# Performance work log

Hardware: AMD Instinct MI355X
Metric: run time of the kernel (lower is better)

## Reference

```python
import jax, jax.numpy as jnp
import numpy as np

B, C, H, W = 8, 128, 64, 64
D_STATE = 16
D_CONV = 4
EXPAND = 1.25
D_INNER = int(EXPAND * C)        # 160
DT_RANK = int(np.ceil(C / 16))   # 8


def setup_inputs() -> dict:
    key = jax.random.key(0)
    ks = jax.random.split(key, 10)
    f = lambda k, s, sc=0.02: jax.random.normal(k, s, dtype=jnp.float32) * sc
    return {
        "x": jax.random.normal(ks[0], (B, C, H, W), dtype=jnp.float32),
        "ln_g": jnp.ones((C,), jnp.float32),
        "ln_b": jnp.zeros((C,), jnp.float32),
        "in_proj_w": f(ks[1], (2 * D_INNER, C)),
        "conv_w": f(ks[2], (D_INNER, 1, D_CONV)),            # depthwise causal conv kernel
        "conv_b": jnp.zeros((D_INNER,), jnp.float32),
        "x_proj_w": f(ks[3], (DT_RANK + 2 * D_STATE, D_INNER)),
        "dt_proj_w": f(ks[4], (D_INNER, DT_RANK), 0.1),
        "dt_proj_b": f(ks[5], (D_INNER,), 0.1),
        # S4-style init: A_log = log(1..d_state) per inner channel (frozen in torch module)
        "A_log": jnp.log(jnp.tile(jnp.arange(1, D_STATE + 1, dtype=jnp.float32), (D_INNER, 1))),
        "D_param": jnp.ones((D_INNER,), jnp.float32),
        "out_proj_w": f(ks[6], (C, D_INNER)),
        "fuse_w": f(ks[7], (C, 2 * C)),                      # 1x1 conv == per-token matmul
        "scale": jnp.ones((1,), jnp.float32) * 0.1,
    }


def _layernorm(x, g, b, eps=1e-5):
    m = x.mean(-1, keepdims=True)
    v = x.var(-1, keepdims=True)
    return (x - m) * jax.lax.rsqrt(v + eps) * g + b


def _mamba(seq, in_proj_w, conv_w, conv_b, x_proj_w, dt_proj_w, dt_proj_b,
           A_log, D_param, out_proj_w):
    # seq: (B, L, C)
    Bsz, L, _ = seq.shape
    xz = jnp.einsum('blc,ec->ble', seq, in_proj_w)           # (B, L, 2*d_inner)
    xm, z = jnp.split(xz, 2, axis=-1)
    # depthwise causal conv over L, truncated to L (padding = d_conv-1 on the left)
    xc = jax.lax.conv_general_dilated(
        xm.transpose(0, 2, 1), conv_w, (1,), [(D_CONV - 1, 0)],
        feature_group_count=D_INNER, dimension_numbers=('NCH', 'OIH', 'NCH'))
    xm = jax.nn.silu((xc + conv_b[None, :, None]).transpose(0, 2, 1))  # (B, L, d_inner)
    x_dbl = jnp.einsum('bld,ed->ble', xm, x_proj_w)
    dt = x_dbl[..., :DT_RANK]
    Bm = x_dbl[..., DT_RANK:DT_RANK + D_STATE]               # (B, L, d_state)
    Cm = x_dbl[..., DT_RANK + D_STATE:]                      # (B, L, d_state)
    dt = jax.nn.softplus(jnp.einsum('blr,dr->bld', dt, dt_proj_w) + dt_proj_b)
    A = -jnp.exp(A_log)                                      # (d_inner, d_state)

    def step(h, inp):
        dt_t, B_t, C_t, x_t = inp                            # (B,d) (B,n) (B,n) (B,d)
        dA = jnp.exp(dt_t[:, :, None] * A)                   # (B, d_inner, d_state)
        h = dA * h + (dt_t * x_t)[:, :, None] * B_t[:, None, :]
        y = jnp.einsum('bdn,bn->bd', h, C_t)
        return h, y

    h0 = jnp.zeros((Bsz, D_INNER, D_STATE), dtype=seq.dtype)
    xs = (dt.transpose(1, 0, 2), Bm.transpose(1, 0, 2),
          Cm.transpose(1, 0, 2), xm.transpose(1, 0, 2))
    _, ys = jax.lax.scan(step, h0, xs)                       # ys: (L, B, d_inner)
    y = ys.transpose(1, 0, 2) + xm * D_param
    y = y * jax.nn.silu(z)
    return jnp.einsum('bld,cd->blc', y, out_proj_w)          # (B, L, C)


def reference(x, ln_g, ln_b, in_proj_w, conv_w, conv_b, x_proj_w, dt_proj_w,
              dt_proj_b, A_log, D_param, out_proj_w, fuse_w, scale):
    Bsz, Ch, Hh, Ww = x.shape
    seq = x.reshape(Bsz, Ch, Hh * Ww).transpose(0, 2, 1)     # (B, L, C) raster order
    seq_n = _layernorm(seq, ln_g, ln_b)                      # LN is per-token: commutes with flip
    args = (in_proj_w, conv_w, conv_b, x_proj_w, dt_proj_w, dt_proj_b,
            A_log, D_param, out_proj_w)
    y0 = _mamba(seq_n, *args)                                # forward raster scan
    y1 = _mamba(seq_n[:, ::-1, :], *args)[:, ::-1, :]        # reversed raster scan
    fused = jnp.einsum('blk,ck->blc', jnp.concatenate([y0, y1], axis=-1), fuse_w)
    out = seq + scale * fused                                # residual + learned scale
    return out.transpose(0, 2, 1).reshape(Bsz, Ch, Hh, Ww)
```

## Files before the change

kernel.cpp:

```cpp
#include <hip/hip_runtime.h>
#include <math.h>

#define LSEQ   4096
#define BATCH  8
#define CDIM   128
#define DIN    160
#define DSTATE 16
#define DTRANK 8
#define BLROWS (BATCH*LSEQ)
#define NCHUNK 128
#define TCH    32
#define SUBC   8
#define NSEG   16

typedef __attribute__((ext_vector_type(8))) short short8;
typedef __attribute__((ext_vector_type(8))) __bf16 bf16x8;
typedef __attribute__((ext_vector_type(4))) float float4v;

__device__ __forceinline__ float4v mfma_bf16(short8 a, short8 b, float4v c) {
  return __builtin_amdgcn_mfma_f32_16x16x32_bf16(
      __builtin_bit_cast(bf16x8, a), __builtin_bit_cast(bf16x8, b), c, 0, 0, 0);
}

__device__ __forceinline__ unsigned short f2bf(float f) {
  union { float f; unsigned u; } v; v.f = f;
  unsigned r = v.u + 0x7FFF + ((v.u >> 16) & 1);
  return (unsigned short)(r >> 16);
}
__device__ __forceinline__ float bf2f(unsigned short h) {
  union { unsigned u; float f; } v; v.u = ((unsigned)h) << 16;
  return v.f;
}

__global__ void prep_weights(const float* __restrict__ inpw, const float* __restrict__ xpw,
                             const float* __restrict__ fuse_w, const float* __restrict__ out_proj_w,
                             unsigned short* __restrict__ inpw_bf, unsigned short* __restrict__ xpw_bf,
                             unsigned short* __restrict__ W01) {
  int i = blockIdx.x * 256 + threadIdx.x;
  if (i < 320 * 128) inpw_bf[i] = f2bf(inpw[i]);
  if (i < 40 * 160)  xpw_bf[i]  = f2bf(xpw[i]);
  if (i < CDIM * DIN) {
    int d = i % DIN, c = i / DIN;
    float a0 = 0.f, a1 = 0.f;
    for (int k = 0; k < CDIM; ++k) {
      float o = out_proj_w[k * DIN + d];
      a0 += fuse_w[c * 256 + k] * o;
      a1 += fuse_w[c * 256 + 128 + k] * o;
    }
    W01[c * DIN + d] = f2bf(a0);
    W01[CDIM * DIN + c * DIN + d] = f2bf(a1);
  }
}

__global__ void ln_transpose_kernel(const float* __restrict__ x,
                                    const float* __restrict__ g,
                                    const float* __restrict__ bb,
                                    unsigned short* __restrict__ seqn) {
  __shared__ float sA[128 * 65];
  __shared__ float psum[2 * 256];
  __shared__ float mrs[2 * 64];
  int l0 = blockIdx.x * 64;
  int b  = blockIdx.y;
  int t  = threadIdx.x;
  int lsub = t & 63, crow = t >> 6;
  const float* xb = x + (size_t)b * CDIM * LSEQ;
  for (int it = 0; it < 32; ++it) {
    int c = crow + it * 4;
    sA[c * 65 + lsub] = xb[(size_t)c * LSEQ + l0 + lsub];
  }
  __syncthreads();
  float s = 0.f, ss = 0.f;
  for (int j = 0; j < 32; ++j) {
    int c = crow * 32 + j;
    float v = sA[c * 65 + lsub];
    s += v; ss += v * v;
  }
  psum[crow * 64 + lsub] = s;
  psum[256 + crow * 64 + lsub] = ss;
  __syncthreads();
  if (t < 64) {
    float su = 0.f, sq = 0.f;
    for (int p = 0; p < 4; ++p) { su += psum[p * 64 + t]; sq += psum[256 + p * 64 + t]; }
    float m = su * (1.f / 128.f);
    float var = sq * (1.f / 128.f) - m * m;
    mrs[t] = m;
    mrs[64 + t] = rsqrtf(var + 1e-5f);
  }
  __syncthreads();
  int c = t & 127, half = t >> 7;
  float gc = g[c], bc = bb[c];
  for (int it = 0; it < 32; ++it) {
    int l = it * 2 + half;
    float v = (sA[c * 65 + l] - mrs[l]) * mrs[64 + l] * gc + bc;
    seqn[((size_t)(b * LSEQ + l0 + l)) * CDIM + c] = f2bf(v);
  }
}

template<int K, bool MASKN, bool BF16OUT>
__global__ __launch_bounds__(256)
void gemm_mfma(const unsigned short* __restrict__ A0, const unsigned short* __restrict__ A1,
               const unsigned short* __restrict__ W,
               void* __restrict__ C0, void* __restrict__ C1, int N) {
  constexpr int LSTR = K + 8;
  __shared__ __align__(16) unsigned short As[64 * LSTR];
  __shared__ __align__(16) unsigned short Ws[64 * LSTR];
  const unsigned short* A = blockIdx.z ? A1 : A0;
  void* Cp = blockIdx.z ? C1 : C0;
  int m0 = blockIdx.x * 64;
  int n0 = blockIdx.y * 64;
  int t = threadIdx.x;
  constexpr int CH = 64 * K / 8;
  for (int c = t; c < CH; c += 256) {
    int row = c / (K / 8);
    int col = (c % (K / 8)) * 8;
    *(short8*)&As[row * LSTR + col] = *(const short8*)&A[(size_t)(m0 + row) * K + col];
    short8 wv = {};
    int nr = n0 + row;
    if (!MASKN || nr < N) wv = *(const short8*)&W[(size_t)nr * K + col];
    *(short8*)&Ws[row * LSTR + col] = wv;
  }
  __syncthreads();
  int lane = t & 63;
  int w = t >> 6;
  int l15 = lane & 15, quad = lane >> 4;
  float4v acc[4] = {};
#pragma unroll
  for (int kk = 0; kk < K; kk += 32) {
    short8 bfrag = *(const short8*)&Ws[(w * 16 + l15) * LSTR + kk + quad * 8];
#pragma unroll
    for (int i = 0; i < 4; ++i) {
      short8 afrag = *(const short8*)&As[(i * 16 + l15) * LSTR + kk + quad * 8];
      acc[i] = mfma_bf16(afrag, bfrag, acc[i]);
    }
  }
  int col = n0 + w * 16 + l15;
  if (MASKN && col >= N) return;
#pragma unroll
  for (int i = 0; i < 4; ++i)
#pragma unroll
    for (int r = 0; r < 4; ++r) {
      int row = m0 + i * 16 + quad * 4 + r;
      if (BF16OUT) ((unsigned short*)Cp)[(size_t)row * N + col] = f2bf(acc[i][r]);
      else         ((float*)Cp)[(size_t)row * N + col] = acc[i][r];
    }
}

__global__ void conv_silu_kernel(const unsigned short* __restrict__ xz,
                                 const float* __restrict__ cw,
                                 const float* __restrict__ cb,
                                 unsigned short* __restrict__ xm0,
                                 unsigned short* __restrict__ xm1) {
  int idx = blockIdx.x * 256 + threadIdx.x;
  int dir = blockIdx.y;
  if (idx >= BLROWS * 80) return;
  int dp = idx % 80;
  int bl = idx / 80;
  int l = bl % LSEQ, b = bl / LSEQ;
  int d = dp * 2;
  float w0[4], w1[4];
#pragma unroll
  for (int k = 0; k < 4; ++k) { w0[k] = cw[d * 4 + k]; w1[k] = cw[d * 4 + 4 + k]; }
  float a0 = cb[d], a1 = cb[d + 1];
  const unsigned short* base = xz + ((size_t)b * LSEQ) * 320 + d;
  if (dir == 0) {
#pragma unroll
    for (int k = 0; k < 4; ++k) {
      int lp = l - 3 + k;
      if (lp >= 0) {
        unsigned v = *(const unsigned*)&base[(size_t)lp * 320];
        a0 += w0[k] * bf2f((unsigned short)v);
        a1 += w1[k] * bf2f((unsigned short)(v >> 16));
      }
    }
  } else {
#pragma unroll
    for (int k = 0; k < 4; ++k) {
      int lp = l + 3 - k;
      if (lp < LSEQ) {
        unsigned v = *(const unsigned*)&base[(size_t)lp * 320];
        a0 += w0[k] * bf2f((unsigned short)v);
        a1 += w1[k] * bf2f((unsigned short)(v >> 16));
      }
    }
  }
  float s0 = a0 / (1.f + __expf(-a0));
  float s1 = a1 / (1.f + __expf(-a1));
  unsigned outv = (unsigned)f2bf(s0) | ((unsigned)f2bf(s1) << 16);
  unsigned short* xm = dir ? xm1 : xm0;
  *(unsigned*)&xm[(size_t)bl * DIN + d] = outv;
}

__device__ __forceinline__ void decay_powers(float r1, float* dA) {
  float r2 = r1 * r1;
  float r4 = r2 * r2;
  float r8 = r4 * r4;
  dA[0] = r1;       dA[1] = r2;       dA[2] = r2 * r1;  dA[3] = r4;
  dA[4] = r4 * r1;  dA[5] = r4 * r2;  dA[6] = r4 * dA[2]; dA[7] = r8;
  dA[8] = r8 * r1;  dA[9] = r8 * r2;  dA[10] = r8 * dA[2]; dA[11] = r8 * r4;
  dA[12] = r8 * dA[4]; dA[13] = r8 * dA[5]; dA[14] = r8 * dA[6]; dA[15] = r8 * r8;
}

__device__ __forceinline__ const float* uniform_row(const float* base, int elem_off) {
  return base + __builtin_amdgcn_readfirstlane(elem_off);
}

__global__ void scan_passA(const float* __restrict__ xdbl0, const float* __restrict__ xdbl1,
                           const unsigned short* __restrict__ xm0v, const unsigned short* __restrict__ xm1v,
                           const float* __restrict__ dt_w, const float* __restrict__ dt_b,
                           const float* __restrict__ Dp,
                           float* __restrict__ Q, float* __restrict__ dtsum,
                           _Float16* __restrict__ rc0, _Float16* __restrict__ rc1,
                           unsigned short* __restrict__ y0, unsigned short* __restrict__ y1) {
  int chunk = blockIdx.x, b = blockIdx.y, dir = blockIdx.z;
  int t = threadIdx.x;
  if (t >= DIN) return;
  const float* xdbl = dir ? xdbl1 : xdbl0;
  const unsigned short* xm = dir ? xm1v : xm0v;
  _Float16* rc = dir ? rc1 : rc0;
  unsigned short* yl = dir ? y1 : y0;
  int d = t;
  float dw[8];
#pragma unroll
  for (int r = 0; r < 8; ++r) dw[r] = dt_w[d * 8 + r];
  float db = dt_b[d];
  float Dd = Dp[d];
  float h[16];
#pragma unroll
  for (int n = 0; n < 16; ++n) h[n] = 0.f;
  float cum = 0.f;
  float rcum = 1.f;
#pragma unroll 4
  for (int tt = 0; tt < TCH; ++tt) {
    int pos = chunk * TCH + tt;
    int l = dir ? (LSEQ - 1 - pos) : pos;
    int rowi = b * LSEQ + l;
    const float* xr = uniform_row(xdbl, rowi * 40);
    float xmv = bf2f(xm[(size_t)rowi * DIN + d]);
    float zz = db;
#pragma unroll
    for (int r = 0; r < 8; ++r) zz += xr[r] * dw[r];
    float e  = __expf(fminf(zz, 20.f));
    float dt = (zz > 20.f) ? zz : __logf(1.f + e);
    float r1 = 1.f / (1.f + e);
    cum += dt;
    rcum *= r1;
    rc[(size_t)rowi * DIN + d] = (_Float16)rcum;
    float u = dt * xmv;
    float dA[16];
    decay_powers(r1, dA);
    float y = xmv * Dd;
#pragma unroll
    for (int n = 0; n < 16; ++n) {
      h[n] = dA[n] * h[n] + u * xr[8 + n];
      y += h[n] * xr[24 + n];
    }
    yl[(size_t)rowi * DIN + d] = f2bf(y);
  }
  size_t base = (size_t)((dir * BATCH + b) * NCHUNK + chunk);
#pragma unroll
  for (int n = 0; n < 16; ++n) Q[base * (DIN * 16) + d * 16 + n] = h[n];
  dtsum[base * DIN + d] = cum;
}

__global__ __launch_bounds__(256)
void scan_passB(const float* __restrict__ Q, const float* __restrict__ dtsum,
                float* __restrict__ Hinit) {
  __shared__ float sA[NSEG * 16], sQ[NSEG * 16];
  int blk = blockIdx.x;
  int d = blk % DIN;
  int rem = blk / DIN;
  int t = threadIdx.x;
  int n = t & 15, cs = t >> 4;
  float An = -(float)(n + 1);
  float a[SUBC], q[SUBC];
  float Aseg = 1.f, Qseg = 0.f;
#pragma unroll
  for (int j = 0; j < SUBC; ++j) {
    int ch = cs * SUBC + j;
    size_t base = (size_t)rem * NCHUNK + ch;
    float dsv = dtsum[base * DIN + d];
    float av = __expf(An * dsv);
    float qv = Q[base * (DIN * 16) + d * 16 + n];
    a[j] = av; q[j] = qv;
    Qseg = av * Qseg + qv;
    Aseg *= av;
  }
  sA[cs * 16 + n] = Aseg;
  sQ[cs * 16 + n] = Qseg;
  __syncthreads();
  if (t < 16) {
    float h = 0.f;
    for (int s = 0; s < NSEG; ++s) {
      float Av = sA[s * 16 + t], Qv = sQ[s * 16 + t];
      sA[s * 16 + t] = h;
      h = Av * h + Qv;
    }
  }
  __syncthreads();
  float h = sA[cs * 16 + n];
#pragma unroll
  for (int j = 0; j < SUBC; ++j) {
    int ch = cs * SUBC + j;
    size_t base = (size_t)rem * NCHUNK + ch;
    Hinit[base * (DIN * 16) + d * 16 + n] = h;
    h = a[j] * h + q[j];
  }
}

__global__ void scan_passC(const float* __restrict__ xdbl0, const float* __restrict__ xdbl1,
                           const unsigned short* __restrict__ xz,
                           const float* __restrict__ Hinit,
                           const _Float16* __restrict__ rc0, const _Float16* __restrict__ rc1,
                           const unsigned short* __restrict__ yl0, const unsigned short* __restrict__ yl1,
                           unsigned short* __restrict__ yg0, unsigned short* __restrict__ yg1) {
  int chunk = blockIdx.x, b = blockIdx.y, dir = blockIdx.z;
  int t = threadIdx.x;
  if (t >= DIN) return;
  const float* xdbl = dir ? xdbl1 : xdbl0;
  const _Float16* rc = dir ? rc1 : rc0;
  const unsigned short* yl = dir ? yl1 : yl0;
  unsigned short* yg = dir ? yg1 : yg0;
  int d = t;
  size_t base = (size_t)((dir * BATCH + b) * NCHUNK + chunk);
  float H0[16];
#pragma unroll
  for (int n = 0; n < 16; ++n) H0[n] = Hinit[base * (DIN * 16) + d * 16 + n];
#pragma unroll 2
  for (int tt = 0; tt < TCH; ++tt) {
    int pos = chunk * TCH + tt;
    int l = dir ? (LSEQ - 1 - pos) : pos;
    int rowi = b * LSEQ + l;
    const float* xr = uniform_row(xdbl, rowi * 40 + 24);
    size_t di = (size_t)rowi * DIN + d;
    float y = bf2f(yl[di]);
    float rcum = (float)rc[di];
    float zv = bf2f(xz[(size_t)rowi * 320 + 160 + d]);
    float dA[16];
    decay_powers(rcum, dA);
    float corr = 0.f;
#pragma unroll
    for (int n = 0; n < 16; ++n) corr += xr[n] * dA[n] * H0[n];
    y += corr;
    float sz = zv / (1.f + __expf(-zv));
    yg[di] = f2bf(y * sz);
  }
}

__global__ __launch_bounds__(256)
void final_mfma(const unsigned short* __restrict__ yg0, const unsigned short* __restrict__ yg1,
                const unsigned short* __restrict__ W01, const float* __restrict__ x,
                const float* __restrict__ scale, float* __restrict__ out) {
  constexpr int K = DIN, LSTR = K + 8;
  __shared__ __align__(16) unsigned short As[64 * LSTR];
  __shared__ __align__(16) unsigned short Ws[64 * LSTR];
  float* sC = (float*)As;
  int m0 = blockIdx.x * 64;
  int c0 = blockIdx.y * 64;
  int b = m0 / LSEQ, l0 = m0 % LSEQ;
  int t = threadIdx.x;
  int lane = t & 63;
  int w = t >> 6;
  int l15 = lane & 15, quad = lane >> 4;
  float4v acc[4] = {};
  for (int pass = 0; pass < 2; ++pass) {
    const unsigned short* A = pass ? yg1 : yg0;
    const unsigned short* W = W01 + pass * (CDIM * K);
    if (pass) __syncthreads();
    constexpr int CH = 64 * K / 8;
    for (int c = t; c < CH; c += 256) {
      int row = c / (K / 8);
      int col = (c % (K / 8)) * 8;
      *(short8*)&As[row * LSTR + col] = *(const short8*)&A[(size_t)(m0 + row) * K + col];
      *(short8*)&Ws[row * LSTR + col] = *(const short8*)&W[(size_t)(c0 + row) * K + col];
    }
    __syncthreads();
#pragma unroll
    for (int kk = 0; kk < K; kk += 32) {
      short8 bfrag = *(const short8*)&Ws[(w * 16 + l15) * LSTR + kk + quad * 8];
#pragma unroll
      for (int i = 0; i < 4; ++i) {
        short8 afrag = *(const short8*)&As[(i * 16 + l15) * LSTR + kk + quad * 8];
        acc[i] = mfma_bf16(afrag, bfrag, acc[i]);
      }
    }
  }
  __syncthreads();
#pragma unroll
  for (int i = 0; i < 4; ++i)
#pragma unroll
    for (int r = 0; r < 4; ++r)
      sC[(i * 16 + quad * 4 + r) * 65 + w * 16 + l15] = acc[i][r];
  __syncthreads();
  float sc = scale[0];
  int ll = t & 63, cq = t >> 6;
#pragma unroll
  for (int j = 0; j < 16; ++j) {
    int cl = cq * 16 + j;
    float v = sC[ll * 65 + cl];
    size_t gi = ((size_t)(b * CDIM + c0 + cl)) * LSEQ + l0 + ll;
    out[gi] = x[gi] + sc * v;
  }
}

extern "C" void kernel_launch(void* const* d_in, const int* in_sizes, int n_in,
                              void* d_out, int out_size, void* d_ws, size_t ws_size,
                              hipStream_t stream) {
  const float* x        = (const float*)d_in[0];
  const float* ln_g     = (const float*)d_in[1];
  const float* ln_b     = (const float*)d_in[2];
  const float* in_projw = (const float*)d_in[3];
  const float* conv_w   = (const float*)d_in[4];
  const float* conv_b   = (const float*)d_in[5];
  const float* x_projw  = (const float*)d_in[6];
  const float* dt_projw = (const float*)d_in[7];
  const float* dt_projb = (const float*)d_in[8];
  const float* A_log    = (const float*)d_in[9];
  const float* D_param  = (const float*)d_in[10];
  const float* out_projw= (const float*)d_in[11];
  const float* fuse_w   = (const float*)d_in[12];
  const float* scale    = (const float*)d_in[13];
  float* out = (float*)d_out;
  (void)A_log;

  float* ws = (float*)d_ws;
  size_t off = 0;
  unsigned short* seqn_bf = (unsigned short*)(ws + off); off += (size_t)BLROWS * CDIM / 2;
  unsigned short* xz      = (unsigned short*)(ws + off); off += (size_t)BLROWS * 320 / 2;
  unsigned short* xm0 = (unsigned short*)(ws + off); off += (size_t)BLROWS * DIN / 2;
  unsigned short* xm1 = (unsigned short*)(ws + off); off += (size_t)BLROWS * DIN / 2;
  float* xdbl0 = ws + off; off += (size_t)BLROWS * 40;
  float* xdbl1 = ws + off; off += (size_t)BLROWS * 40;
  float* Q     = ws + off; off += (size_t)2 * BATCH * NCHUNK * DIN * 16;
  float* Hinit = ws + off; off += (size_t)2 * BATCH * NCHUNK * DIN * 16;
  float* dtsum = ws + off; off += (size_t)2 * BATCH * NCHUNK * DIN;
  _Float16* rc0 = (_Float16*)(ws + off); off += (size_t)BLROWS * DIN / 2;
  _Float16* rc1 = (_Float16*)(ws + off); off += (size_t)BLROWS * DIN / 2;
  unsigned short* yl0 = (unsigned short*)(ws + off); off += (size_t)BLROWS * DIN / 2;
  unsigned short* yl1 = (unsigned short*)(ws + off); off += (size_t)BLROWS * DIN / 2;
  unsigned short* yg0 = (unsigned short*)(ws + off); off += (size_t)BLROWS * DIN / 2;
  unsigned short* yg1 = (unsigned short*)(ws + off); off += (size_t)BLROWS * DIN / 2;
  unsigned short* W01bf = (unsigned short*)(ws + off); off += (size_t)2 * CDIM * DIN / 2;
  unsigned short* inpw_bf = (unsigned short*)(ws + off); off += (size_t)320 * 128 / 2;
  unsigned short* xpw_bf  = (unsigned short*)(ws + off); off += (size_t)40 * 160 / 2 + 8;

  prep_weights<<<(320 * 128 + 255) / 256, 256, 0, stream>>>(
      in_projw, x_projw, fuse_w, out_projw, inpw_bf, xpw_bf, W01bf);
  ln_transpose_kernel<<<dim3(LSEQ / 64, BATCH), 256, 0, stream>>>(x, ln_g, ln_b, seqn_bf);
  gemm_mfma<128, false, true><<<dim3(BLROWS / 64, 5, 1), 256, 0, stream>>>(
      seqn_bf, seqn_bf, inpw_bf, xz, xz, 320);
  conv_silu_kernel<<<dim3((BLROWS * 80 + 255) / 256, 2), 256, 0, stream>>>(xz, conv_w, conv_b, xm0, xm1);
  gemm_mfma<160, true, false><<<dim3(BLROWS / 64, 1, 2), 256, 0, stream>>>(
      xm0, xm1, xpw_bf, xdbl0, xdbl1, 40);
  scan_passA<<<dim3(NCHUNK, BATCH, 2), 192, 0, stream>>>(xdbl0, xdbl1, xm0, xm1,
                                                         dt_projw, dt_projb, D_param,
                                                         Q, dtsum, rc0, rc1, yl0, yl1);
  scan_passB<<<2 * BATCH * DIN, 256, 0, stream>>>(Q, dtsum, Hinit);
  scan_passC<<<dim3(NCHUNK, BATCH, 2), 192, 0, stream>>>(xdbl0, xdbl1, xz, Hinit,
                                                         rc0, rc1, yl0, yl1, yg0, yg1);
  final_mfma<<<dim3(BLROWS / 64, CDIM / 64), 256, 0, stream>>>(yg0, yg1, W01bf, x, scale, out);
}
```

Measured before the change: 249.0 us.

## Halve scan chunk length, store chunk states in bf16, split correction reduction

Doubles the number of scan chunks (16 steps each instead of 32) so pass A and pass C launch twice as many blocks and each thread runs a shorter serial loop. Per-chunk end states Q and carried-in states Hinit are now stored as bf16 instead of fp32, which offsets the doubled state traffic. Pass C's 16-term correction sum is split into four independent accumulators to shorten the dependency chain. The cost is more inter-chunk state passing in pass B (16 sub-chunks per segment) and extra rounding error in the carried scan states.

```diff
diff --git a/kernel.cpp b/kernel.cpp
--- a/kernel.cpp
+++ b/kernel.cpp
@@ -8,9 +8,9 @@
 #define DSTATE 16
 #define DTRANK 8
 #define BLROWS (BATCH*LSEQ)
-#define NCHUNK 128
-#define TCH    32
-#define SUBC   8
+#define NCHUNK 256
+#define TCH    16
+#define SUBC   16
 #define NSEG   16
 
 typedef __attribute__((ext_vector_type(8))) short short8;
@@ -208,16 +208,16 @@
                            const unsigned short* __restrict__ xm0v, const unsigned short* __restrict__ xm1v,
                            const float* __restrict__ dt_w, const float* __restrict__ dt_b,
                            const float* __restrict__ Dp,
-                           float* __restrict__ Q, float* __restrict__ dtsum,
+                           unsigned short* __restrict__ Q, float* __restrict__ dtsum,
                            _Float16* __restrict__ rc0, _Float16* __restrict__ rc1,
-                           unsigned short* __restrict__ y0, unsigned short* __restrict__ y1) {
+                           unsigned short* __restrict__ y0out, unsigned short* __restrict__ y1out) {
   int chunk = blockIdx.x, b = blockIdx.y, dir = blockIdx.z;
   int t = threadIdx.x;
   if (t >= DIN) return;
   const float* xdbl = dir ? xdbl1 : xdbl0;
   const unsigned short* xm = dir ? xm1v : xm0v;
   _Float16* rc = dir ? rc1 : rc0;
-  unsigned short* yl = dir ? y1 : y0;
+  unsigned short* yl = dir ? y1out : y0out;
   int d = t;
   float dw[8];
 #pragma unroll
@@ -258,13 +258,13 @@
   }
   size_t base = (size_t)((dir * BATCH + b) * NCHUNK + chunk);
 #pragma unroll
-  for (int n = 0; n < 16; ++n) Q[base * (DIN * 16) + d * 16 + n] = h[n];
+  for (int n = 0; n < 16; ++n) Q[base * (DIN * 16) + d * 16 + n] = f2bf(h[n]);
   dtsum[base * DIN + d] = cum;
 }
 
 __global__ __launch_bounds__(256)
-void scan_passB(const float* __restrict__ Q, const float* __restrict__ dtsum,
-                float* __restrict__ Hinit) {
+void scan_passB(const unsigned short* __restrict__ Q, const float* __restrict__ dtsum,
+                unsigned short* __restrict__ Hinit) {
   __shared__ float sA[NSEG * 16], sQ[NSEG * 16];
   int blk = blockIdx.x;
   int d = blk % DIN;
@@ -280,7 +280,7 @@
     size_t base = (size_t)rem * NCHUNK + ch;
     float dsv = dtsum[base * DIN + d];
     float av = __expf(An * dsv);
-    float qv = Q[base * (DIN * 16) + d * 16 + n];
+    float qv = bf2f(Q[base * (DIN * 16) + d * 16 + n]);
     a[j] = av; q[j] = qv;
     Qseg = av * Qseg + qv;
     Aseg *= av;
@@ -302,14 +302,14 @@
   for (int j = 0; j < SUBC; ++j) {
     int ch = cs * SUBC + j;
     size_t base = (size_t)rem * NCHUNK + ch;
-    Hinit[base * (DIN * 16) + d * 16 + n] = h;
+    Hinit[base * (DIN * 16) + d * 16 + n] = f2bf(h);
     h = a[j] * h + q[j];
   }
 }
 
 __global__ void scan_passC(const float* __restrict__ xdbl0, const float* __restrict__ xdbl1,
                            const unsigned short* __restrict__ xz,
-                           const float* __restrict__ Hinit,
+                           const unsigned short* __restrict__ Hinit,
                            const _Float16* __restrict__ rc0, const _Float16* __restrict__ rc1,
                            const unsigned short* __restrict__ yl0, const unsigned short* __restrict__ yl1,
                            unsigned short* __restrict__ yg0, unsigned short* __restrict__ yg1) {
@@ -324,7 +324,7 @@
   size_t base = (size_t)((dir * BATCH + b) * NCHUNK + chunk);
   float H0[16];
 #pragma unroll
-  for (int n = 0; n < 16; ++n) H0[n] = Hinit[base * (DIN * 16) + d * 16 + n];
+  for (int n = 0; n < 16; ++n) H0[n] = bf2f(Hinit[base * (DIN * 16) + d * 16 + n]);
 #pragma unroll 2
   for (int tt = 0; tt < TCH; ++tt) {
     int pos = chunk * TCH + tt;
@@ -337,10 +337,15 @@
     float zv = bf2f(xz[(size_t)rowi * 320 + 160 + d]);
     float dA[16];
     decay_powers(rcum, dA);
-    float corr = 0.f;
-#pragma unroll
-    for (int n = 0; n < 16; ++n) corr += xr[n] * dA[n] * H0[n];
-    y += corr;
+    float c0 = 0.f, c1 = 0.f, c2 = 0.f, c3 = 0.f;
+#pragma unroll
+    for (int n = 0; n < 4; ++n) {
+      c0 += xr[n]      * dA[n]      * H0[n];
+      c1 += xr[n + 4]  * dA[n + 4]  * H0[n + 4];
+      c2 += xr[n + 8]  * dA[n + 8]  * H0[n + 8];
+      c3 += xr[n + 12] * dA[n + 12] * H0[n + 12];
+    }
+    y += (c0 + c1) + (c2 + c3);
     float sz = zv / (1.f + __expf(-zv));
     yg[di] = f2bf(y * sz);
   }
@@ -430,8 +435,8 @@
   unsigned short* xm1 = (unsigned short*)(ws + off); off += (size_t)BLROWS * DIN / 2;
   float* xdbl0 = ws + off; off += (size_t)BLROWS * 40;
   float* xdbl1 = ws + off; off += (size_t)BLROWS * 40;
-  float* Q     = ws + off; off += (size_t)2 * BATCH * NCHUNK * DIN * 16;
-  float* Hinit = ws + off; off += (size_t)2 * BATCH * NCHUNK * DIN * 16;
+  unsigned short* Q     = (unsigned short*)(ws + off); off += (size_t)2 * BATCH * NCHUNK * DIN * 16 / 2;
+  unsigned short* Hinit = (unsigned short*)(ws + off); off += (size_t)2 * BATCH * NCHUNK * DIN * 16 / 2;
   float* dtsum = ws + off; off += (size_t)2 * BATCH * NCHUNK * DIN;
   _Float16* rc0 = (_Float16*)(ws + off); off += (size_t)BLROWS * DIN / 2;
   _Float16* rc1 = (_Float16*)(ws + off); off += (size_t)BLROWS * DIN / 2;
```

Measured after the change: 251.7 us. No clear change (+1.1%).
